# Optimization experiments

Hardware: AMD Instinct MI355X
Metric: run time of the kernel (lower is better)

The kernel has to match this reference:

```python
import jax, jax.numpy as jnp
import numpy as np

IOU_THRESH = 0.5
IMG = 640.0


def _cxcywh_to_xyxy(b):
    cx, cy, w, h = b[:, 0], b[:, 1], b[:, 2], b[:, 3]
    return jnp.stack([cx - w * 0.5, cy - h * 0.5, cx + w * 0.5, cy + h * 0.5], axis=1)


def _iou_matrix(b):
    # b: [N,4] xyxy -> [N,N] IoU
    x1, y1, x2, y2 = b[:, 0], b[:, 1], b[:, 2], b[:, 3]
    area = (x2 - x1) * (y2 - y1)
    iw = jnp.maximum(jnp.minimum(x2[:, None], x2[None, :]) - jnp.maximum(x1[:, None], x1[None, :]), 0.0)
    ih = jnp.maximum(jnp.minimum(y2[:, None], y2[None, :]) - jnp.maximum(y1[:, None], y1[None, :]), 0.0)
    inter = iw * ih
    union = area[:, None] + area[None, :] - inter
    return inter / jnp.maximum(union, 1e-9)


def _nms_keep(xyxy_sorted):
    # greedy NMS over score-descending boxes; returns bool keep mask [N]
    iou = jax.lax.stop_gradient(_iou_matrix(xyxy_sorted))
    n = xyxy_sorted.shape[0]
    idx = jnp.arange(n)

    def body(i, keep):
        sup = keep[i] & (iou[i] > IOU_THRESH) & (idx > i)
        return keep & ~sup

    keep = jax.lax.fori_loop(0, n, body, jnp.ones((n,), dtype=bool))
    return jax.lax.stop_gradient(keep)


def setup_inputs() -> dict:
    key = jax.random.key(0)
    k1, k2, k3, k4 = jax.random.split(key, 4)

    def boxes(k, n):
        u = jax.random.uniform(k, (n, 4), dtype=jnp.float32)
        centers = u[:, :2] * IMG                 # cx, cy in [0, 640)
        wh = 4.0 + u[:, 2:] * 96.0               # w, h in [4, 100)
        return jnp.concatenate([centers, wh], axis=1)

    return {
        "yolo_cxcywh": boxes(k1, 8400),
        "yolo_person_conf": jax.random.uniform(k2, (8400,), dtype=jnp.float32),
        "rtdetr_cxcywh": boxes(k3, 300),
        "rtdetr_person_conf": jax.random.uniform(k4, (300,), dtype=jnp.float32),
    }


def reference(yolo_cxcywh, yolo_person_conf, rtdetr_cxcywh, rtdetr_person_conf):
    cxcywh = jnp.concatenate([yolo_cxcywh, rtdetr_cxcywh], axis=0)
    conf = jnp.concatenate([
        jnp.clip(yolo_person_conf, 0.0, 1.0),
        jnp.clip(rtdetr_person_conf, 0.0, 1.0),
    ], axis=0)
    xyxy = _cxcywh_to_xyxy(cxcywh)
    # torchvision.ops.nms processes boxes in score-descending order and
    # returns kept indices in that order; we emit a fixed-shape [N,5] array
    # sorted by score with suppressed rows zeroed (jit-compatible equivalent).
    order = jnp.argsort(-conf)
    xyxy_s = xyxy[order]
    conf_s = conf[order]
    keep = _nms_keep(xyxy_s)
    boxes_and_scores = jnp.concatenate([xyxy_s, conf_s[:, None]], axis=1)
    return boxes_and_scores * keep[:, None].astype(boxes_and_scores.dtype)
```

## Files before the change

### kernel.cpp

```cpp
#include <hip/hip_runtime.h>

typedef unsigned long long u64;
typedef unsigned int u32;

#define MAXN 8704
#define CHUNK 512
#define RSTRIDE 192
#define ITCAP 8704

__global__ void prep_kernel(const float* __restrict__ yb, const float* __restrict__ yc,
                            const float* __restrict__ db, const float* __restrict__ dc,
                            int n1, int n,
                            float4* __restrict__ xyxy, float* __restrict__ conf,
                            u32* __restrict__ key) {
    int i = blockIdx.x * 256 + threadIdx.x;
    if (i >= n) return;
    float cx, cy, w, h, c;
    if (i < n1) {
        const float* b = yb + (size_t)i * 4;
        cx = b[0]; cy = b[1]; w = b[2]; h = b[3]; c = yc[i];
    } else {
        const float* b = db + (size_t)(i - n1) * 4;
        cx = b[0]; cy = b[1]; w = b[2]; h = b[3]; c = dc[i - n1];
    }
    c = fminf(fmaxf(c, 0.0f), 1.0f);
    float hw = w * 0.5f, hh = h * 0.5f;
    xyxy[i] = make_float4(cx - hw, cy - hh, cx + hw, cy + hh);
    conf[i] = c;
    key[i]  = __float_as_uint(c);
}

__global__ void rank_kernel(const u32* __restrict__ key, int n, int* __restrict__ rank) {
    __shared__ __align__(16) u32 sk[CHUNK];
    int t = threadIdx.x;
    int jbase = blockIdx.y * CHUNK;
    for (int s = t; s < CHUNK; s += 256) {
        int j = jbase + s;
        sk[s] = (j < n) ? key[j] : 0u;
    }
    __syncthreads();
    int i = blockIdx.x * 256 + t;
    if (i >= n) return;
    u32 ki = key[i];
    int cnt = 0;
    const uint4* sk4 = (const uint4*)sk;
    for (int s = 0; s < CHUNK / 4; ++s) {
        uint4 k = sk4[s];
        int j = jbase + s * 4;
        cnt += (k.x > ki) || (k.x == ki && (j + 0) < i);
        cnt += (k.y > ki) || (k.y == ki && (j + 1) < i);
        cnt += (k.z > ki) || (k.z == ki && (j + 2) < i);
        cnt += (k.w > ki) || (k.w == ki && (j + 3) < i);
    }
    if (cnt) atomicAdd(&rank[i], cnt);
}

__global__ void scatter_kernel(const float4* __restrict__ xyxy, const float* __restrict__ conf,
                               const int* __restrict__ rank, int n,
                               float4* __restrict__ sbox, float* __restrict__ sconf) {
    int i = blockIdx.x * 256 + threadIdx.x;
    if (i >= n) return;
    int r = rank[i];
    sbox[r]  = xyxy[i];
    sconf[r] = conf[i];
}

__global__ void iou_kernel(const float4* __restrict__ sbox, int n, int nw,
                           u64* __restrict__ sup) {
    int bi = blockIdx.y, bj = blockIdx.x;
    if (bj < bi) return;
    __shared__ float4 cb[64];
    int t  = threadIdx.x;
    int j0 = bj * 64;
    int jt = j0 + t;
    cb[t] = (jt < n) ? sbox[jt] : make_float4(0, 0, 0, 0);
    __syncthreads();
    int i = bi * 64 + t;
    if (i >= n) return;
    float4 a = sbox[i];
    float areaA = (a.z - a.x) * (a.w - a.y);
    u64 word = 0;
    int kmax = min(64, n - j0);
    for (int k = 0; k < kmax; ++k) {
        int j = j0 + k;
        float4 b = cb[k];
        float iw = fmaxf(fminf(a.z, b.z) - fmaxf(a.x, b.x), 0.0f);
        float ih = fmaxf(fminf(a.w, b.w) - fmaxf(a.y, b.y), 0.0f);
        float inter = iw * ih;
        float areaB = (b.z - b.x) * (b.w - b.y);
        float uni = areaA + areaB - inter;
        float iou = inter / fmaxf(uni, 1e-9f);
        if (j > i && iou > 0.5f) word |= (1ULL << k);
    }
    sup[(size_t)i * nw + bj] = word;
}

__device__ __forceinline__ void gather_group(const u64* __restrict__ sup, int nw, int n,
                                             int wg, u64 kw, int wv, int l,
                                             u64& a0, u64& a1, u64& a2) {
    int rb = wg << 6;
    int r0 = rb + (wv << 4);
    bool g0 = (l >= wg)        && (l < nw);
    bool g1 = (l + 64 >= wg)   && (l + 64 < nw);
    bool g2 = (l + 128 >= wg)  && (l + 128 < nw);
    for (int i = 0; i < 16; ++i) {
        int r = r0 + i;
        if (r < n && ((kw >> ((wv << 4) + i)) & 1)) {
            const u64* __restrict__ row = sup + (size_t)r * nw;
            if (g0) a0 |= row[l];
            if (g1) a1 |= row[l + 64];
            if (g2) a2 |= row[l + 128];
        }
    }
}

__global__ __launch_bounds__(256) void nms_jacobi(const u64* __restrict__ sup,
                                                  const float* __restrict__ sbox,
                                                  const float* __restrict__ sconf,
                                                  int n, int nw,
                                                  u64* __restrict__ remv3,
                                                  int* __restrict__ bar,
                                                  float* __restrict__ out,
                                                  int nblk) {
    __shared__ u64 s_part[4][RSTRIDE];
    __shared__ u64 s_cur[RSTRIDE];

    int t  = threadIdx.x;
    int g  = blockIdx.x;
    int wA = g, wB = nw - 1 - g;
    int wv = t >> 6, l = t & 63;

    u64 prevW = ~0ull;
    u64 mPrev = 0;
    u64 pkA = 0, pkB = 0;

    for (int it = 0;; ++it) {
        u64* cur = remv3 + (size_t)(it % 3) * RSTRIDE;
        u64* nxt = remv3 + (size_t)((it + 1) % 3) * RSTRIDE;
        u64* zz  = remv3 + (size_t)((it + 2) % 3) * RSTRIDE;

        int mydiff = 0;
        if (t < nw) {
            u64 c = __hip_atomic_load(&cur[t], __ATOMIC_ACQUIRE, __HIP_MEMORY_SCOPE_AGENT);
            s_cur[t] = c;
            mydiff = (c != prevW);
            prevW = c;
            __hip_atomic_store(&zz[t], (u64)0, __ATOMIC_RELAXED, __HIP_MEMORY_SCOPE_AGENT);
        }
        int changed = __syncthreads_or(mydiff);

        if (!changed || it == ITCAP) {
            for (int e = t; e < 640; e += 256) {
                int grp = (e >= 320);
                int ee  = e - grp * 320;
                int i   = ee / 5;
                int c   = ee - i * 5;
                int wg  = grp ? wB : wA;
                int r   = (wg << 6) + i;
                if (r < n) {
                    float keep = ((s_cur[wg] >> i) & 1) ? 0.0f : 1.0f;
                    float v = (c < 4) ? sbox[(size_t)r * 4 + c] : sconf[r];
                    out[(size_t)r * 5 + c] = v * keep;
                }
            }
            return;
        }

        u64 kA = ~s_cur[wA];
        u64 kB = ~s_cur[wB];
        bool redo = (kA != pkA) || (kB != pkB);
        if (redo) {
            u64 a0 = 0, a1 = 0, a2 = 0;
            gather_group(sup, nw, n, wA, kA, wv, l, a0, a1, a2);
            if (wB != wA) gather_group(sup, nw, n, wB, kB, wv, l, a0, a1, a2);
            s_part[wv][l]       = a0;
            s_part[wv][l + 64]  = a1;
            s_part[wv][l + 128] = a2;
            __syncthreads();
            if (t < nw) {
                mPrev = s_part[0][t] | s_part[1][t] | s_part[2][t] | s_part[3][t];
            }
        }
        pkA = kA; pkB = kB;

        if (t < nw && mPrev)
            atomicOr((unsigned long long*)&nxt[t], (unsigned long long)mPrev);

        __threadfence();
        __syncthreads();
        if (t == 0) {
            int target = it + 1;
            int prev = __hip_atomic_fetch_add(&bar[0], 1, __ATOMIC_ACQ_REL, __HIP_MEMORY_SCOPE_AGENT);
            if (prev == nblk * target - 1) {
                __hip_atomic_store(&bar[1], target, __ATOMIC_RELEASE, __HIP_MEMORY_SCOPE_AGENT);
            } else {
                while (__hip_atomic_load(&bar[1], __ATOMIC_ACQUIRE, __HIP_MEMORY_SCOPE_AGENT) < target)
                    __builtin_amdgcn_s_sleep(4);
            }
        }
        __syncthreads();
    }
}

extern "C" void kernel_launch(void* const* d_in, const int* in_sizes, int n_in,
                              void* d_out, int out_size, void* d_ws, size_t ws_size,
                              hipStream_t stream) {
    const float* yb = (const float*)d_in[0];
    const float* yc = (const float*)d_in[1];
    const float* db = (const float*)d_in[2];
    const float* dc = (const float*)d_in[3];
    int n1 = in_sizes[1];
    int n2 = in_sizes[3];
    int n  = n1 + n2;
    int nw = (n + 63) / 64;

    char* w = (char*)d_ws;
    u64*    sup   = (u64*)w;
    float4* xyxy  = (float4*)(w + (size_t)MAXN * nw * 8);
    float4* sbox  = xyxy + MAXN;
    float*  conf  = (float*)(sbox + MAXN);
    float*  sconf = conf + MAXN;
    u32*    key   = (u32*)(sconf + MAXN);
    int*    rank  = (int*)(key + MAXN);
    u64*    remv3 = (u64*)(rank + MAXN);
    int*    bar   = (int*)(remv3 + 3 * RSTRIDE);

    hipMemsetAsync(rank, 0, MAXN * sizeof(int), stream);
    hipMemsetAsync(remv3, 0, 3 * RSTRIDE * sizeof(u64) + 2 * sizeof(int), stream);

    int nb = (n + 255) / 256;
    prep_kernel<<<nb, 256, 0, stream>>>(yb, yc, db, dc, n1, n, xyxy, conf, key);

    dim3 g1(nb, (n + CHUNK - 1) / CHUNK);
    rank_kernel<<<g1, 256, 0, stream>>>(key, n, rank);

    scatter_kernel<<<nb, 256, 0, stream>>>(xyxy, conf, rank, n, sbox, sconf);

    dim3 g3(nw, nw);
    iou_kernel<<<g3, 64, 0, stream>>>(sbox, n, nw, sup);

    int nblk = (nw + 1) / 2;
    nms_jacobi<<<nblk, 256, 0, stream>>>(sup, (const float*)sbox, sconf, n, nw,
                                         remv3, bar, (float*)d_out, nblk);
}
```

Baseline: 293.8 us.

## Restructure Jacobi NMS grid barrier with per-block partials and flag arrays

Each block of the iterative NMS kernel now handles four 64-box words with 512 threads instead of two words with 256 threads, which halves the block count. The shared atomicOr-reduced suppression buffer is replaced by per-block partial arrays that every block reads and reduces. The counter-based grid barrier is replaced by per-block padded arrival slots polled in parallel, plus a rotating convergence flag. The memsets are folded into the prep kernel, and the gather loop is unrolled and made branchless. The goal is lower per-iteration barrier and atomic latency and fewer launches, at the cost of more global reads per iteration and reliance on nw being divisible by 4.

```diff
diff --git a/kernel.cpp b/kernel.cpp
--- a/kernel.cpp
+++ b/kernel.cpp
@@ -6,14 +6,18 @@
 #define MAXN 8704
 #define CHUNK 512
 #define RSTRIDE 192
+#define ARRPAD 16
 #define ITCAP 8704
 
 __global__ void prep_kernel(const float* __restrict__ yb, const float* __restrict__ yc,
                             const float* __restrict__ db, const float* __restrict__ dc,
                             int n1, int n,
                             float4* __restrict__ xyxy, float* __restrict__ conf,
-                            u32* __restrict__ key) {
+                            u32* __restrict__ key, int* __restrict__ rank,
+                            int* __restrict__ ctrl) {
     int i = blockIdx.x * 256 + threadIdx.x;
+    if (i < MAXN) rank[i] = 0;
+    if (i < 1024) ctrl[i] = 0;
     if (i >= n) return;
     float cx, cy, w, h, c;
     if (i < n1) {
@@ -95,70 +99,70 @@
     sup[(size_t)i * nw + bj] = word;
 }
 
-__device__ __forceinline__ void gather_group(const u64* __restrict__ sup, int nw, int n,
-                                             int wg, u64 kw, int wv, int l,
-                                             u64& a0, u64& a1, u64& a2) {
-    int rb = wg << 6;
-    int r0 = rb + (wv << 4);
-    bool g0 = (l >= wg)        && (l < nw);
-    bool g1 = (l + 64 >= wg)   && (l + 64 < nw);
-    bool g2 = (l + 128 >= wg)  && (l + 128 < nw);
-    for (int i = 0; i < 16; ++i) {
-        int r = r0 + i;
-        if (r < n && ((kw >> ((wv << 4) + i)) & 1)) {
-            const u64* __restrict__ row = sup + (size_t)r * nw;
-            if (g0) a0 |= row[l];
-            if (g1) a1 |= row[l + 64];
-            if (g2) a2 |= row[l + 128];
-        }
-    }
-}
-
-__global__ __launch_bounds__(256) void nms_jacobi(const u64* __restrict__ sup,
+__global__ __launch_bounds__(512) void nms_jacobi(const u64* __restrict__ sup,
                                                   const float* __restrict__ sbox,
                                                   const float* __restrict__ sconf,
                                                   int n, int nw,
-                                                  u64* __restrict__ remv3,
-                                                  int* __restrict__ bar,
-                                                  float* __restrict__ out,
-                                                  int nblk) {
-    __shared__ u64 s_part[4][RSTRIDE];
-    __shared__ u64 s_cur[RSTRIDE];
-
-    int t  = threadIdx.x;
-    int g  = blockIdx.x;
-    int wA = g, wB = nw - 1 - g;
-    int wv = t >> 6, l = t & 63;
-
-    u64 prevW = ~0ull;
-    u64 mPrev = 0;
-    u64 pkA = 0, pkB = 0;
+                                                  u64* __restrict__ partial,
+                                                  int* __restrict__ ctrl,
+                                                  float* __restrict__ out) {
+    __shared__ u64 s_part[8][RSTRIDE];
+    __shared__ u64 s_new[4];
+    __shared__ u64 s_prevw[4];
+    __shared__ int s_fl;
+
+    const int t    = threadIdx.x;
+    const int g    = blockIdx.x;
+    const int nblk = gridDim.x;
+    const int Wq[4] = {2 * g, 2 * g + 1, nw - 2 - 2 * g, nw - 1 - 2 * g};
+
+    const int sg    = t >> 6;
+    const int l     = t & 63;
+    const int gq    = sg >> 1;
+    const int wg    = Wq[gq];
+    const int rbase = wg * 64 + (sg & 1) * 32;
+    const int shft  = (sg & 1) * 32;
+    const bool b0 = (l >= wg);
+    const bool b1 = (l + 64 >= wg);
+    const bool b2 = (l + 128 >= wg) && (l + 128 < nw);
+    const u64 M0 = b0 ? ~0ull : 0ull;
+    const u64 M1 = b1 ? ~0ull : 0ull;
+    const u64 M2 = b2 ? ~0ull : 0ull;
+    const int cc0 = b0 ? l : wg;
+    const int cc1 = b1 ? l + 64 : wg;
+    const int cc2 = b2 ? l + 128 : nw - 1;
+
+    const int rq = t / nblk;
+    const int rp = t - rq * nblk;
+
+    int* arrv = ctrl;
+    int* flag = ctrl + 64 * ARRPAD;
+
+    if (t < 4) s_prevw[t] = ~0ull;
+
+    u64 pword = 0;
 
     for (int it = 0;; ++it) {
-        u64* cur = remv3 + (size_t)(it % 3) * RSTRIDE;
-        u64* nxt = remv3 + (size_t)((it + 1) % 3) * RSTRIDE;
-        u64* zz  = remv3 + (size_t)((it + 2) % 3) * RSTRIDE;
-
-        int mydiff = 0;
-        if (t < nw) {
-            u64 c = __hip_atomic_load(&cur[t], __ATOMIC_ACQUIRE, __HIP_MEMORY_SCOPE_AGENT);
-            s_cur[t] = c;
-            mydiff = (c != prevW);
-            prevW = c;
-            __hip_atomic_store(&zz[t], (u64)0, __ATOMIC_RELAXED, __HIP_MEMORY_SCOPE_AGENT);
-        }
-        int changed = __syncthreads_or(mydiff);
-
-        if (!changed || it == ITCAP) {
-            for (int e = t; e < 640; e += 256) {
-                int grp = (e >= 320);
-                int ee  = e - grp * 320;
-                int i   = ee / 5;
-                int c   = ee - i * 5;
-                int wg  = grp ? wB : wA;
-                int r   = (wg << 6) + i;
+        if (t < 4) s_new[t] = 0;
+        if (t == 0) s_fl = (it > 0)
+            ? __hip_atomic_load(&flag[(it - 1) & 3], __ATOMIC_RELAXED, __HIP_MEMORY_SCOPE_AGENT)
+            : 1;
+        __syncthreads();
+        if (it > 0 && t < 4 * nblk) {
+            u64 v = __hip_atomic_load(&partial[(size_t)(1 - (it & 1)) * nblk * RSTRIDE +
+                                               (size_t)rp * RSTRIDE + Wq[rq]],
+                                      __ATOMIC_RELAXED, __HIP_MEMORY_SCOPE_AGENT);
+            if (v) atomicOr(&s_new[rq], v);
+        }
+        __syncthreads();
+
+        if (s_fl == 0 || it >= ITCAP) {
+            for (int e = t; e < 1280; e += 512) {
+                int qq = e / 320, ee = e - qq * 320;
+                int i = ee / 5, c = ee - i * 5;
+                int r = Wq[qq] * 64 + i;
                 if (r < n) {
-                    float keep = ((s_cur[wg] >> i) & 1) ? 0.0f : 1.0f;
+                    float keep = ((s_new[qq] >> i) & 1) ? 0.0f : 1.0f;
                     float v = (c < 4) ? sbox[(size_t)r * 4 + c] : sconf[r];
                     out[(size_t)r * 5 + c] = v * keep;
                 }
@@ -166,39 +170,55 @@
             return;
         }
 
-        u64 kA = ~s_cur[wA];
-        u64 kB = ~s_cur[wB];
-        bool redo = (kA != pkA) || (kB != pkB);
-        if (redo) {
+        int d = 0;
+        if (t < 4) { d = (s_new[t] != s_prevw[t]); s_prevw[t] = s_new[t]; }
+        int ch = __syncthreads_or(d);
+
+        if (t == 0) {
+            if (ch) atomicOr(&flag[it & 3], 1);
+            if (g == 0)
+                __hip_atomic_store(&flag[(it + 2) & 3], 0, __ATOMIC_RELAXED, __HIP_MEMORY_SCOPE_AGENT);
+        }
+
+        if (ch) {
+            const u64 kwv = ~s_new[gq];
             u64 a0 = 0, a1 = 0, a2 = 0;
-            gather_group(sup, nw, n, wA, kA, wv, l, a0, a1, a2);
-            if (wB != wA) gather_group(sup, nw, n, wB, kB, wv, l, a0, a1, a2);
-            s_part[wv][l]       = a0;
-            s_part[wv][l + 64]  = a1;
-            s_part[wv][l + 128] = a2;
+            #pragma unroll
+            for (int i = 0; i < 32; ++i) {
+                int r = rbase + i;
+                const u64* __restrict__ row = sup + (size_t)min(r, n - 1) * nw;
+                u64 m = (((kwv >> (shft + i)) & 1) && (r < n)) ? ~0ull : 0ull;
+                a0 |= row[cc0] & (m & M0);
+                a1 |= row[cc1] & (m & M1);
+                a2 |= row[cc2] & (m & M2);
+            }
+            s_part[sg][l]       = a0;
+            s_part[sg][l + 64]  = a1;
+            s_part[sg][l + 128] = a2;
             __syncthreads();
             if (t < nw) {
-                mPrev = s_part[0][t] | s_part[1][t] | s_part[2][t] | s_part[3][t];
+                u64 v = 0;
+                #pragma unroll
+                for (int s = 0; s < 8; ++s) v |= s_part[s][t];
+                pword = v;
             }
         }
-        pkA = kA; pkB = kB;
-
-        if (t < nw && mPrev)
-            atomicOr((unsigned long long*)&nxt[t], (unsigned long long)mPrev);
+        if (t < nw)
+            __hip_atomic_store(&partial[(size_t)(it & 1) * nblk * RSTRIDE +
+                                        (size_t)g * RSTRIDE + t],
+                               pword, __ATOMIC_RELAXED, __HIP_MEMORY_SCOPE_AGENT);
 
         __threadfence();
         __syncthreads();
-        if (t == 0) {
-            int target = it + 1;
-            int prev = __hip_atomic_fetch_add(&bar[0], 1, __ATOMIC_ACQ_REL, __HIP_MEMORY_SCOPE_AGENT);
-            if (prev == nblk * target - 1) {
-                __hip_atomic_store(&bar[1], target, __ATOMIC_RELEASE, __HIP_MEMORY_SCOPE_AGENT);
-            } else {
-                while (__hip_atomic_load(&bar[1], __ATOMIC_ACQUIRE, __HIP_MEMORY_SCOPE_AGENT) < target)
-                    __builtin_amdgcn_s_sleep(4);
-            }
-        }
-        __syncthreads();
+        if (t == 0)
+            __hip_atomic_store(&arrv[g * ARRPAD], it + 1, __ATOMIC_RELEASE, __HIP_MEMORY_SCOPE_AGENT);
+        int ok;
+        do {
+            ok = (t < nblk)
+               ? (__hip_atomic_load(&arrv[t * ARRPAD], __ATOMIC_RELAXED, __HIP_MEMORY_SCOPE_AGENT) >= it + 1)
+               : 1;
+        } while (!__syncthreads_and(ok));
+        __threadfence();
     }
 }
 
@@ -213,23 +233,21 @@
     int n2 = in_sizes[3];
     int n  = n1 + n2;
     int nw = (n + 63) / 64;
+    int nblk = nw / 4;
 
     char* w = (char*)d_ws;
-    u64*    sup   = (u64*)w;
-    float4* xyxy  = (float4*)(w + (size_t)MAXN * nw * 8);
-    float4* sbox  = xyxy + MAXN;
-    float*  conf  = (float*)(sbox + MAXN);
-    float*  sconf = conf + MAXN;
-    u32*    key   = (u32*)(sconf + MAXN);
-    int*    rank  = (int*)(key + MAXN);
-    u64*    remv3 = (u64*)(rank + MAXN);
-    int*    bar   = (int*)(remv3 + 3 * RSTRIDE);
-
-    hipMemsetAsync(rank, 0, MAXN * sizeof(int), stream);
-    hipMemsetAsync(remv3, 0, 3 * RSTRIDE * sizeof(u64) + 2 * sizeof(int), stream);
+    u64*    sup     = (u64*)w;
+    float4* xyxy    = (float4*)(w + (size_t)MAXN * nw * 8);
+    float4* sbox    = xyxy + MAXN;
+    float*  conf    = (float*)(sbox + MAXN);
+    float*  sconf   = conf + MAXN;
+    u32*    key     = (u32*)(sconf + MAXN);
+    int*    rank    = (int*)(key + MAXN);
+    u64*    partial = (u64*)(rank + MAXN);
+    int*    ctrl    = (int*)(partial + (size_t)2 * nblk * RSTRIDE);
 
     int nb = (n + 255) / 256;
-    prep_kernel<<<nb, 256, 0, stream>>>(yb, yc, db, dc, n1, n, xyxy, conf, key);
+    prep_kernel<<<nb, 256, 0, stream>>>(yb, yc, db, dc, n1, n, xyxy, conf, key, rank, ctrl);
 
     dim3 g1(nb, (n + CHUNK - 1) / CHUNK);
     rank_kernel<<<g1, 256, 0, stream>>>(key, n, rank);
@@ -239,7 +257,6 @@
     dim3 g3(nw, nw);
     iou_kernel<<<g3, 64, 0, stream>>>(sbox, n, nw, sup);
 
-    int nblk = (nw + 1) / 2;
-    nms_jacobi<<<nblk, 256, 0, stream>>>(sup, (const float*)sbox, sconf, n, nw,
-                                         remv3, bar, (float*)d_out, nblk);
-}
+    nms_jacobi<<<nblk, 512, 0, stream>>>(sup, (const float*)sbox, sconf, n, nw,
+                                         partial, ctrl, (float*)d_out);
+}
```

Result: faster. 276.0 us (-6.1%).

## Replace multi-block Jacobi NMS with single-block pipelined sequential scan

Applied to the files above, without the earlier changes.

Swaps the iterative multi-block Jacobi fixed-point NMS, which needs a grid-wide atomic barrier on every iteration, for a single 512-thread block that scans the 64-box words in order. Within each word a wave resolves the keep mask using lane reads, and suppression rows for the next words are prefetched into registers while the far-future OR updates are deferred by one phase. The rank reset moves into the prep kernel, removing the memsets. The cost is that all the sequential NMS work now runs on one CU with about 132 dependent phases, each ending in a __syncthreads.

```diff
diff --git a/kernel.cpp b/kernel.cpp
--- a/kernel.cpp
+++ b/kernel.cpp
@@ -5,15 +5,22 @@
 
 #define MAXN 8704
 #define CHUNK 512
-#define RSTRIDE 192
-#define ITCAP 8704
+#define SMAX 6
+
+__device__ inline u64 shfl_xor_u64(u64 v, int m) {
+    u32 lo = (u32)v, hi = (u32)(v >> 32);
+    lo = (u32)__shfl_xor((int)lo, m, 64);
+    hi = (u32)__shfl_xor((int)hi, m, 64);
+    return ((u64)hi << 32) | lo;
+}
 
 __global__ void prep_kernel(const float* __restrict__ yb, const float* __restrict__ yc,
                             const float* __restrict__ db, const float* __restrict__ dc,
                             int n1, int n,
                             float4* __restrict__ xyxy, float* __restrict__ conf,
-                            u32* __restrict__ key) {
+                            u32* __restrict__ key, int* __restrict__ rank) {
     int i = blockIdx.x * 256 + threadIdx.x;
+    if (i < MAXN) rank[i] = 0;
     if (i >= n) return;
     float cx, cy, w, h, c;
     if (i < n1) {
@@ -95,110 +102,151 @@
     sup[(size_t)i * nw + bj] = word;
 }
 
-__device__ __forceinline__ void gather_group(const u64* __restrict__ sup, int nw, int n,
-                                             int wg, u64 kw, int wv, int l,
-                                             u64& a0, u64& a1, u64& a2) {
-    int rb = wg << 6;
-    int r0 = rb + (wv << 4);
-    bool g0 = (l >= wg)        && (l < nw);
-    bool g1 = (l + 64 >= wg)   && (l + 64 < nw);
-    bool g2 = (l + 128 >= wg)  && (l + 128 < nw);
-    for (int i = 0; i < 16; ++i) {
-        int r = r0 + i;
-        if (r < n && ((kw >> ((wv << 4) + i)) & 1)) {
-            const u64* __restrict__ row = sup + (size_t)r * nw;
-            if (g0) a0 |= row[l];
-            if (g1) a1 |= row[l + 64];
-            if (g2) a2 |= row[l + 128];
-        }
-    }
-}
-
-__global__ __launch_bounds__(256) void nms_jacobi(const u64* __restrict__ sup,
-                                                  const float* __restrict__ sbox,
-                                                  const float* __restrict__ sconf,
-                                                  int n, int nw,
-                                                  u64* __restrict__ remv3,
-                                                  int* __restrict__ bar,
-                                                  float* __restrict__ out,
-                                                  int nblk) {
-    __shared__ u64 s_part[4][RSTRIDE];
-    __shared__ u64 s_cur[RSTRIDE];
-
-    int t  = threadIdx.x;
-    int g  = blockIdx.x;
-    int wA = g, wB = nw - 1 - g;
-    int wv = t >> 6, l = t & 63;
-
-    u64 prevW = ~0ull;
-    u64 mPrev = 0;
-    u64 pkA = 0, pkB = 0;
-
-    for (int it = 0;; ++it) {
-        u64* cur = remv3 + (size_t)(it % 3) * RSTRIDE;
-        u64* nxt = remv3 + (size_t)((it + 1) % 3) * RSTRIDE;
-        u64* zz  = remv3 + (size_t)((it + 2) % 3) * RSTRIDE;
-
-        int mydiff = 0;
-        if (t < nw) {
-            u64 c = __hip_atomic_load(&cur[t], __ATOMIC_ACQUIRE, __HIP_MEMORY_SCOPE_AGENT);
-            s_cur[t] = c;
-            mydiff = (c != prevW);
-            prevW = c;
-            __hip_atomic_store(&zz[t], (u64)0, __ATOMIC_RELAXED, __HIP_MEMORY_SCOPE_AGENT);
-        }
-        int changed = __syncthreads_or(mydiff);
-
-        if (!changed || it == ITCAP) {
-            for (int e = t; e < 640; e += 256) {
-                int grp = (e >= 320);
-                int ee  = e - grp * 320;
-                int i   = ee / 5;
-                int c   = ee - i * 5;
-                int wg  = grp ? wB : wA;
-                int r   = (wg << 6) + i;
-                if (r < n) {
-                    float keep = ((s_cur[wg] >> i) & 1) ? 0.0f : 1.0f;
-                    float v = (c < 4) ? sbox[(size_t)r * 4 + c] : sconf[r];
-                    out[(size_t)r * 5 + c] = v * keep;
+template<int PW>
+__device__ __forceinline__ void phase_step(
+    int p, int n, int nw, const u64* __restrict__ sup, int t,
+    u64* s_remv, u64* s_kws, u32 (*s_klist)[64], int* s_kcnt, int* s_lg,
+    u64& BUj0, u64& BUj1, u64& BUj2, u64& BUj3,
+    u64& BIj0, u64& BIj1, u64& BIj2, u64& BIj3,
+    u64 (&FV)[SMAX], int (&FT)[SMAX])
+{
+    constexpr int PR = PW ^ 1;
+    #pragma unroll
+    for (int i = 0; i < SMAX; ++i)
+        if (FT[i] >= 0) atomicOr(&s_remv[FT[i]], FV[i]);
+
+    if (t < 64) {
+        int rem = n - (p << 6);
+        u64 vm = (rem >= 64) ? ~0ull : (rem <= 0 ? 0ull : ((1ull << rem) - 1ull));
+        u64 cand = ~s_remv[p] & vm;
+        u64 kw = 0;
+        u32 dlo = (u32)BUj0, dhi = (u32)(BUj0 >> 32);
+        while (cand) {
+            int k1 = __builtin_amdgcn_readfirstlane((int)__builtin_ctzll(cand));
+            u64 s1 = (((u64)(u32)__builtin_amdgcn_readlane((int)dhi, k1)) << 32)
+                   |  ((u64)(u32)__builtin_amdgcn_readlane((int)dlo, k1));
+            u64 c1 = cand & ~(1ull << k1);
+            kw |= 1ull << k1;
+            if (c1) {
+                int k2 = __builtin_amdgcn_readfirstlane((int)__builtin_ctzll(c1));
+                u64 s2 = (((u64)(u32)__builtin_amdgcn_readlane((int)dhi, k2)) << 32)
+                       |  ((u64)(u32)__builtin_amdgcn_readlane((int)dlo, k2));
+                if (!((s1 >> k2) & 1ull)) {
+                    kw |= 1ull << k2;
+                    cand = c1 & ~(1ull << k2) & ~(s1 | s2);
+                } else {
+                    cand = c1 & ~s1;
+                }
+            } else cand = 0;
+        }
+        if (t == 0) s_kws[p] = kw;
+        int kc = __popcll(kw);
+        if ((kw >> t) & 1ull)
+            s_klist[PW][__popcll(kw & ((1ull << t) - 1ull))] = (u32)t;
+        int lg = (kc <= 1) ? 0 : (32 - __builtin_clz(kc - 1));
+        int lastl = 63 - __clzll(kw | 1ull);
+        if (t >= kc && t < (1 << lg)) s_klist[PW][t] = (u32)lastl;
+        if (t == 0) { s_kcnt[PW] = kc; s_lg[PW] = lg; }
+        u64 mm = ((kw >> t) & 1ull) ? ~0ull : 0ull;
+        u64 r1 = BUj1 & mm, r2 = BUj2 & mm, r3 = BUj3 & mm;
+        #pragma unroll
+        for (int m = 1; m < 64; m <<= 1) {
+            r1 |= shfl_xor_u64(r1, m);
+            r2 |= shfl_xor_u64(r2, m);
+            r3 |= shfl_xor_u64(r3, m);
+        }
+        if (t == 0) {
+            if (p + 1 < nw) atomicOr(&s_remv[p + 1], r1);
+            if (p + 2 < nw) atomicOr(&s_remv[p + 2], r2);
+            if (p + 3 < nw) atomicOr(&s_remv[p + 3], r3);
+        }
+        int cc = p + 2;
+        size_t rr = (size_t)min(cc * 64 + t, n - 1) * (size_t)nw;
+        BIj0 = sup[rr + min(cc,     nw - 1)];
+        BIj1 = sup[rr + min(cc + 1, nw - 1)];
+        BIj2 = sup[rr + min(cc + 2, nw - 1)];
+        BIj3 = sup[rr + min(cc + 3, nw - 1)];
+    }
+    {
+        int q = p - 1;
+        #pragma unroll
+        for (int i = 0; i < SMAX; ++i) FT[i] = -1;
+        if (q >= 0) {
+            int kc = s_kcnt[PR], lg = s_lg[PR];
+            int FW = nw - (q + 4);
+            if (kc > 0 && FW > 0) {
+                int kp = 1 << lg;
+                int pairs = FW << lg;
+                #pragma unroll
+                for (int i = 0; i < SMAX; ++i) {
+                    int idx = t + i * 512;
+                    int cidx = min(idx, pairs - 1);
+                    int w = (q + 4) + (cidx >> lg);
+                    int r = (q << 6) + (int)s_klist[PR][cidx & (kp - 1)];
+                    FV[i] = sup[(size_t)r * nw + w];
+                    FT[i] = (idx < pairs) ? w : -1;
+                }
+                for (int idx = t + SMAX * 512; idx < pairs; idx += 512) {
+                    int w = (q + 4) + (idx >> lg);
+                    int r = (q << 6) + (int)s_klist[PR][idx & (kp - 1)];
+                    atomicOr(&s_remv[w], sup[(size_t)r * nw + w]);
                 }
             }
-            return;
-        }
-
-        u64 kA = ~s_cur[wA];
-        u64 kB = ~s_cur[wB];
-        bool redo = (kA != pkA) || (kB != pkB);
-        if (redo) {
-            u64 a0 = 0, a1 = 0, a2 = 0;
-            gather_group(sup, nw, n, wA, kA, wv, l, a0, a1, a2);
-            if (wB != wA) gather_group(sup, nw, n, wB, kB, wv, l, a0, a1, a2);
-            s_part[wv][l]       = a0;
-            s_part[wv][l + 64]  = a1;
-            s_part[wv][l + 128] = a2;
-            __syncthreads();
-            if (t < nw) {
-                mPrev = s_part[0][t] | s_part[1][t] | s_part[2][t] | s_part[3][t];
-            }
-        }
-        pkA = kA; pkB = kB;
-
-        if (t < nw && mPrev)
-            atomicOr((unsigned long long*)&nxt[t], (unsigned long long)mPrev);
-
-        __threadfence();
-        __syncthreads();
-        if (t == 0) {
-            int target = it + 1;
-            int prev = __hip_atomic_fetch_add(&bar[0], 1, __ATOMIC_ACQ_REL, __HIP_MEMORY_SCOPE_AGENT);
-            if (prev == nblk * target - 1) {
-                __hip_atomic_store(&bar[1], target, __ATOMIC_RELEASE, __HIP_MEMORY_SCOPE_AGENT);
-            } else {
-                while (__hip_atomic_load(&bar[1], __ATOMIC_ACQUIRE, __HIP_MEMORY_SCOPE_AGENT) < target)
-                    __builtin_amdgcn_s_sleep(4);
-            }
-        }
-        __syncthreads();
+        }
+    }
+    __syncthreads();
+}
+
+__global__ __launch_bounds__(512) void scan_fs(const u64* __restrict__ sup,
+                                               const float* __restrict__ sbox,
+                                               const float* __restrict__ sconf,
+                                               int n, int nw,
+                                               float* __restrict__ out) {
+    __shared__ u64 s_remv[144];
+    __shared__ u64 s_kws[144];
+    __shared__ u32 s_klist[2][64];
+    __shared__ int s_kcnt[2], s_lg[2];
+
+    int t = threadIdx.x;
+    for (int i = t; i < 144; i += 512) { s_remv[i] = 0; s_kws[i] = 0; }
+    if (t == 0) { s_kcnt[0] = 0; s_kcnt[1] = 0; s_lg[0] = 0; s_lg[1] = 0; }
+
+    u64 B0j0=0,B0j1=0,B0j2=0,B0j3=0;
+    u64 B1j0=0,B1j1=0,B1j2=0,B1j3=0;
+    u64 B2j0=0,B2j1=0,B2j2=0,B2j3=0;
+    u64 FVA[SMAX], FVB[SMAX]; int FTA[SMAX], FTB[SMAX];
+    #pragma unroll
+    for (int i = 0; i < SMAX; ++i) { FTA[i] = -1; FTB[i] = -1; FVA[i] = 0; FVB[i] = 0; }
+
+    if (t < 64) {
+        size_t r0 = (size_t)t * (size_t)nw;
+        B0j0 = sup[r0 + 0]; B0j1 = sup[r0 + 1]; B0j2 = sup[r0 + 2]; B0j3 = sup[r0 + 3];
+        size_t r1 = (size_t)(64 + t) * (size_t)nw;
+        B1j0 = sup[r1 + 1]; B1j1 = sup[r1 + 2]; B1j2 = sup[r1 + 3]; B1j3 = sup[r1 + 4];
+    }
+    __syncthreads();
+
+    int NPH = ((nw + 5) / 6) * 6;
+    for (int pb = 0; pb < NPH; pb += 6) {
+        phase_step<0>(pb+0, n, nw, sup, t, s_remv, s_kws, s_klist, s_kcnt, s_lg,
+                      B0j0,B0j1,B0j2,B0j3, B2j0,B2j1,B2j2,B2j3, FVA, FTA);
+        phase_step<1>(pb+1, n, nw, sup, t, s_remv, s_kws, s_klist, s_kcnt, s_lg,
+                      B1j0,B1j1,B1j2,B1j3, B0j0,B0j1,B0j2,B0j3, FVB, FTB);
+        phase_step<0>(pb+2, n, nw, sup, t, s_remv, s_kws, s_klist, s_kcnt, s_lg,
+                      B2j0,B2j1,B2j2,B2j3, B1j0,B1j1,B1j2,B1j3, FVA, FTA);
+        phase_step<1>(pb+3, n, nw, sup, t, s_remv, s_kws, s_klist, s_kcnt, s_lg,
+                      B0j0,B0j1,B0j2,B0j3, B2j0,B2j1,B2j2,B2j3, FVB, FTB);
+        phase_step<0>(pb+4, n, nw, sup, t, s_remv, s_kws, s_klist, s_kcnt, s_lg,
+                      B1j0,B1j1,B1j2,B1j3, B0j0,B0j1,B0j2,B0j3, FVA, FTA);
+        phase_step<1>(pb+5, n, nw, sup, t, s_remv, s_kws, s_klist, s_kcnt, s_lg,
+                      B2j0,B2j1,B2j2,B2j3, B1j0,B1j1,B1j2,B1j3, FVB, FTB);
+    }
+
+    for (int e = t; e < n * 5; e += 512) {
+        int r = e / 5, c5 = e - r * 5;
+        float keep = ((s_kws[r >> 6] >> (r & 63)) & 1ull) ? 1.0f : 0.0f;
+        float v = (c5 < 4) ? sbox[(size_t)r * 4 + c5] : sconf[r];
+        out[e] = v * keep;
     }
 }
 
@@ -222,14 +270,9 @@
     float*  sconf = conf + MAXN;
     u32*    key   = (u32*)(sconf + MAXN);
     int*    rank  = (int*)(key + MAXN);
-    u64*    remv3 = (u64*)(rank + MAXN);
-    int*    bar   = (int*)(remv3 + 3 * RSTRIDE);
-
-    hipMemsetAsync(rank, 0, MAXN * sizeof(int), stream);
-    hipMemsetAsync(remv3, 0, 3 * RSTRIDE * sizeof(u64) + 2 * sizeof(int), stream);
 
     int nb = (n + 255) / 256;
-    prep_kernel<<<nb, 256, 0, stream>>>(yb, yc, db, dc, n1, n, xyxy, conf, key);
+    prep_kernel<<<nb, 256, 0, stream>>>(yb, yc, db, dc, n1, n, xyxy, conf, key, rank);
 
     dim3 g1(nb, (n + CHUNK - 1) / CHUNK);
     rank_kernel<<<g1, 256, 0, stream>>>(key, n, rank);
@@ -239,7 +282,5 @@
     dim3 g3(nw, nw);
     iou_kernel<<<g3, 64, 0, stream>>>(sbox, n, nw, sup);
 
-    int nblk = (nw + 1) / 2;
-    nms_jacobi<<<nblk, 256, 0, stream>>>(sup, (const float*)sbox, sconf, n, nw,
-                                         remv3, bar, (float*)d_out, nblk);
-}
+    scan_fs<<<1, 512, 0, stream>>>(sup, (const float*)sbox, sconf, n, nw, (float*)d_out);
+}
```

Measured after the change: 890.8 us. 3.03x slower.
